# Kernel optimization log

Measured on AMD Instinct MI355X. Metric: run time of the kernel, lower is better.

## Reference

```python
import jax, jax.numpy as jnp
import numpy as np

NUM_NODES = 50000
NUM_EDGES = 640000
IN_FEAT = 128
OUT_FEAT = 128


def setup_inputs() -> dict:
    key = jax.random.key(0)
    k1, k2, k3, k4 = jax.random.split(key, 4)
    features = jax.random.normal(k1, (NUM_NODES, IN_FEAT), dtype=jnp.float32)
    weight = jax.random.normal(k2, (IN_FEAT, OUT_FEAT), dtype=jnp.float32) * (1.0 / np.sqrt(IN_FEAT))
    edges_dst = jax.random.randint(k3, (NUM_EDGES,), 0, NUM_NODES, dtype=jnp.int32)
    edges_src = jax.random.randint(k4, (NUM_EDGES,), 0, NUM_NODES, dtype=jnp.int32)
    return {"features": features, "weight": weight, "edges_dst": edges_dst, "edges_src": edges_src}


def reference(features, weight, edges_dst, edges_src):
    # nodes_representation = features @ W   -> [N, out_feat]
    nodes_representation = jnp.matmul(features, weight)

    # gather neighbor (source) features: [E, in_feat]
    neighbour = features[edges_src]

    # unsorted_segment_mean over target node ids (edges_dst)
    seg_sum = jax.ops.segment_sum(neighbour, edges_dst, num_segments=NUM_NODES)
    counts = jax.ops.segment_sum(jnp.ones((NUM_EDGES,), dtype=features.dtype),
                                 edges_dst, num_segments=NUM_NODES)
    aggregated = jnp.where(counts[:, None] > 0, seg_sum / jnp.maximum(counts[:, None], 1.0), 0.0)

    aggregated_messages = jnp.matmul(aggregated, weight)  # [N, out_feat]

    # combination_type == 'concat', activation == 'relu'
    h = jnp.concatenate([nodes_representation, aggregated_messages], axis=-1)  # [N, 2*out_feat]
    return jax.nn.relu(h)
```

## Files before the change

### kernel.cpp

```cpp
#include <hip/hip_runtime.h>

#define FEAT 128
#define CAP 64
#define SCAT_BLK 192

typedef __attribute__((ext_vector_type(8))) short bhalf8;
typedef __attribute__((ext_vector_type(4))) float floatx4;

__device__ __forceinline__ unsigned short f2bf(float f) {
    unsigned int u = __float_as_uint(f);
    unsigned int r = (u + 0x7fffu + ((u >> 16) & 1u)) >> 16;
    return (unsigned short)r;
}

#define SB_STRIDE 136
__global__ __launch_bounds__(256, 4) void fused_kernel(
    const float* __restrict__ feat, const float* __restrict__ W,
    unsigned short* __restrict__ P2, float* __restrict__ out, int nrows,
    const int* __restrict__ edst, const int* __restrict__ esrc,
    int* __restrict__ counts, int* __restrict__ bucket, int nE)
{
    __shared__ unsigned short sB[128 * SB_STRIDE];

    const int tid = threadIdx.x;

    if (blockIdx.x < SCAT_BLK) {
        const int nE4 = nE >> 2;
        const int gthreads = SCAT_BLK * 256;
        for (int g = blockIdx.x * 256 + tid; g < nE4; g += gthreads) {
            int4 d = *(const int4*)&edst[g << 2];
            int4 s = *(const int4*)&esrc[g << 2];
            int p;
            p = atomicAdd(&counts[d.x], 1); if (p < CAP) bucket[d.x * CAP + p] = s.x;
            p = atomicAdd(&counts[d.y], 1); if (p < CAP) bucket[d.y * CAP + p] = s.y;
            p = atomicAdd(&counts[d.z], 1); if (p < CAP) bucket[d.z * CAP + p] = s.z;
            p = atomicAdd(&counts[d.w], 1); if (p < CAP) bucket[d.w * CAP + p] = s.w;
        }
        if (blockIdx.x == 0 && tid == 0) {
            for (int i = nE4 << 2; i < nE; ++i) {
                int p = atomicAdd(&counts[edst[i]], 1);
                if (p < CAP) bucket[edst[i] * CAP + p] = esrc[i];
            }
        }
        return;
    }

    const int bx   = blockIdx.x - SCAT_BLK;
    const int wave = tid >> 6;
    const int lane = tid & 63;
    const int m    = lane & 15;
    const int kg   = lane >> 4;

    for (int i = tid; i < 2048; i += 256) {
        int n  = i & 127;
        int kc = i >> 7;
        unsigned short tmp[8];
        #pragma unroll
        for (int t = 0; t < 8; ++t)
            tmp[t] = f2bf(W[(size_t)(kc * 8 + t) * FEAT + n]);
        *(uint4*)&sB[n * SB_STRIDE + kc * 8] = *(uint4*)tmp;
    }

    const int row  = bx * 64 + wave * 16 + m;
    const int rowc = min(row, nrows - 1);
    bhalf8 afrag[4];
    {
        const float* ap = &feat[(size_t)rowc * FEAT + kg * 8];
        #pragma unroll
        for (int ks = 0; ks < 4; ++ks) {
            float4 f0 = *(const float4*)&ap[ks * 32];
            float4 f1 = *(const float4*)&ap[ks * 32 + 4];
            union { bhalf8 v; unsigned short u[8]; } a;
            a.u[0] = f2bf(f0.x); a.u[1] = f2bf(f0.y);
            a.u[2] = f2bf(f0.z); a.u[3] = f2bf(f0.w);
            a.u[4] = f2bf(f1.x); a.u[5] = f2bf(f1.y);
            a.u[6] = f2bf(f1.z); a.u[7] = f2bf(f1.w);
            afrag[ks] = a.v;
        }
    }

    __syncthreads();

    floatx4 acc[8];
    #pragma unroll
    for (int nt = 0; nt < 8; ++nt) acc[nt] = (floatx4){0.f, 0.f, 0.f, 0.f};

    #pragma unroll
    for (int ks = 0; ks < 4; ++ks) {
        #pragma unroll
        for (int nt = 0; nt < 8; ++nt) {
            bhalf8 b = *(bhalf8*)&sB[(nt * 16 + m) * SB_STRIDE + ks * 32 + kg * 8];
            acc[nt] = __builtin_amdgcn_mfma_f32_16x16x32_bf16(afrag[ks], b, acc[nt], 0, 0, 0);
        }
    }

    const int rbase = bx * 64 + wave * 16 + kg * 4;
    #pragma unroll
    for (int i = 0; i < 4; ++i) {
        int r = rbase + i;
        if (r < nrows) {
            #pragma unroll
            for (int nt = 0; nt < 8; ++nt) {
                float v = acc[nt][i];
                int c = nt * 16 + m;
                out[(size_t)r * (2 * FEAT) + c] = fmaxf(v, 0.f);
                P2[(size_t)r * FEAT + c] = f2bf(v);
            }
        }
    }
}

__global__ __launch_bounds__(256) void aggregate_kernel(
    const unsigned short* __restrict__ P2, const int* __restrict__ counts,
    const int* __restrict__ bucket, float* __restrict__ out, int n)
{
    const int node = blockIdx.x * 4 + (threadIdx.x >> 6);
    if (node >= n) return;
    const int lane = threadIdx.x & 63;
    const int g  = lane >> 4;
    const int cl = lane & 15;

    const int deg = min(counts[node], CAP);

    float a[8];
    #pragma unroll
    for (int t = 0; t < 8; ++t) a[t] = 0.f;

    int myIdx = (lane < deg) ? bucket[node * CAP + lane] : 0;

    #pragma unroll 4
    for (int j = 0; j < deg; j += 4) {
        int s = __shfl(myIdx, j + g);
        if (j + g < deg) {
            uint4 v = *(const uint4*)&P2[(size_t)s * FEAT + cl * 8];
            a[0] += __uint_as_float(v.x << 16);
            a[1] += __uint_as_float(v.x & 0xffff0000u);
            a[2] += __uint_as_float(v.y << 16);
            a[3] += __uint_as_float(v.y & 0xffff0000u);
            a[4] += __uint_as_float(v.z << 16);
            a[5] += __uint_as_float(v.z & 0xffff0000u);
            a[6] += __uint_as_float(v.w << 16);
            a[7] += __uint_as_float(v.w & 0xffff0000u);
        }
    }

    #pragma unroll
    for (int t = 0; t < 8; ++t) {
        a[t] += __shfl_xor(a[t], 16);
        a[t] += __shfl_xor(a[t], 32);
    }

    if (g == 0) {
        const float inv = (deg > 0) ? (1.0f / (float)deg) : 0.0f;
        float4 r0 = make_float4(fmaxf(a[0] * inv, 0.f), fmaxf(a[1] * inv, 0.f),
                                fmaxf(a[2] * inv, 0.f), fmaxf(a[3] * inv, 0.f));
        float4 r1 = make_float4(fmaxf(a[4] * inv, 0.f), fmaxf(a[5] * inv, 0.f),
                                fmaxf(a[6] * inv, 0.f), fmaxf(a[7] * inv, 0.f));
        float* op = &out[(size_t)node * (2 * FEAT) + FEAT + cl * 8];
        *(float4*)op = r0;
        *(float4*)(op + 4) = r1;
    }
}

extern "C" void kernel_launch(void* const* d_in, const int* in_sizes, int n_in,
                              void* d_out, int out_size, void* d_ws, size_t ws_size,
                              hipStream_t stream)
{
    const float* feat = (const float*)d_in[0];
    const float* W    = (const float*)d_in[1];
    const int* edst   = (const int*)d_in[2];
    const int* esrc   = (const int*)d_in[3];
    float* out        = (float*)d_out;

    const int N = in_sizes[0] / FEAT;
    const int E = in_sizes[2];

    char* ws = (char*)d_ws;
    unsigned short* P2 = (unsigned short*)ws;
    size_t off = (size_t)N * FEAT * sizeof(unsigned short);
    off = (off + 15) & ~(size_t)15;
    int* counts = (int*)(ws + off); off += (size_t)N * 4;
    off = (off + 15) & ~(size_t)15;
    int* bucket = (int*)(ws + off); off += (size_t)N * CAP * 4;

    hipMemsetAsync(counts, 0, (size_t)N * 4, stream);

    const int gemmBlocks = (N + 63) / 64;
    fused_kernel<<<SCAT_BLK + gemmBlocks, 256, 0, stream>>>(
        feat, W, P2, out, N, edst, esrc, counts, bucket, E);

    aggregate_kernel<<<(N + 3) / 4, 256, 0, stream>>>(P2, counts, bucket, out, N);
}
```

Before: 150.7 us.

## Replace global atomic edge scatter with per-block LDS binning over node ranges

Each binning block now owns a contiguous range of 196 destination nodes. It scans the full edge list, builds counts and source buckets in LDS using shared-memory atomics, then writes them out to global memory with vectorized stores. This removes the contended global atomics, the scattered bucket writes and the counts memset. In exchange, every binning block rereads the whole destination array, so total L2 traffic grows with the number of blocks. The larger shared allocation, now also reserved by the GEMM blocks, may lower occupancy.

```diff
diff --git a/kernel.cpp b/kernel.cpp
--- a/kernel.cpp
+++ b/kernel.cpp
@@ -2,7 +2,8 @@
 
 #define FEAT 128
 #define CAP 64
-#define SCAT_BLK 192
+#define NPB 196
+#define SB_STRIDE 136
 
 typedef __attribute__((ext_vector_type(8))) short bhalf8;
 typedef __attribute__((ext_vector_type(4))) float floatx4;
@@ -13,39 +14,61 @@
     return (unsigned short)r;
 }
 
-#define SB_STRIDE 136
 __global__ __launch_bounds__(256, 4) void fused_kernel(
     const float* __restrict__ feat, const float* __restrict__ W,
     unsigned short* __restrict__ P2, float* __restrict__ out, int nrows,
     const int* __restrict__ edst, const int* __restrict__ esrc,
-    int* __restrict__ counts, int* __restrict__ bucket, int nE)
+    int* __restrict__ counts, int* __restrict__ bucket, int nE, int binBlocks)
 {
-    __shared__ unsigned short sB[128 * SB_STRIDE];
+    __shared__ int4 smem4[(NPB + NPB * CAP) / 4 + 1];
+    int* smem = (int*)smem4;
 
     const int tid = threadIdx.x;
 
-    if (blockIdx.x < SCAT_BLK) {
+    if ((int)blockIdx.x < binBlocks) {
+        int* cnt = smem;
+        int* bkt = smem + NPB;
+        const int base = blockIdx.x * NPB;
+        const unsigned int span = (unsigned int)min(NPB, nrows - base);
+
+        for (int i = tid; i < NPB; i += 256) cnt[i] = 0;
+        __syncthreads();
+
         const int nE4 = nE >> 2;
-        const int gthreads = SCAT_BLK * 256;
-        for (int g = blockIdx.x * 256 + tid; g < nE4; g += gthreads) {
+        for (int g = tid; g < nE4; g += 256) {
             int4 d = *(const int4*)&edst[g << 2];
-            int4 s = *(const int4*)&esrc[g << 2];
-            int p;
-            p = atomicAdd(&counts[d.x], 1); if (p < CAP) bucket[d.x * CAP + p] = s.x;
-            p = atomicAdd(&counts[d.y], 1); if (p < CAP) bucket[d.y * CAP + p] = s.y;
-            p = atomicAdd(&counts[d.z], 1); if (p < CAP) bucket[d.z * CAP + p] = s.z;
-            p = atomicAdd(&counts[d.w], 1); if (p < CAP) bucket[d.w * CAP + p] = s.w;
-        }
-        if (blockIdx.x == 0 && tid == 0) {
-            for (int i = nE4 << 2; i < nE; ++i) {
-                int p = atomicAdd(&counts[edst[i]], 1);
-                if (p < CAP) bucket[edst[i] * CAP + p] = esrc[i];
+            unsigned int l;
+            l = (unsigned int)(d.x - base);
+            if (l < span) { int s = atomicAdd(&cnt[l], 1); if (s < CAP) bkt[l * CAP + s] = esrc[(g << 2) + 0]; }
+            l = (unsigned int)(d.y - base);
+            if (l < span) { int s = atomicAdd(&cnt[l], 1); if (s < CAP) bkt[l * CAP + s] = esrc[(g << 2) + 1]; }
+            l = (unsigned int)(d.z - base);
+            if (l < span) { int s = atomicAdd(&cnt[l], 1); if (s < CAP) bkt[l * CAP + s] = esrc[(g << 2) + 2]; }
+            l = (unsigned int)(d.w - base);
+            if (l < span) { int s = atomicAdd(&cnt[l], 1); if (s < CAP) bkt[l * CAP + s] = esrc[(g << 2) + 3]; }
+        }
+        if (blockIdx.x == 0) {
+            for (int i = (nE4 << 2) + tid; i < nE; i += 256) {
             }
         }
+        for (int i = (nE4 << 2) + tid; i < nE; i += 256) {
+            unsigned int l = (unsigned int)(edst[i] - base);
+            if (l < span) { int s = atomicAdd(&cnt[l], 1); if (s < CAP) bkt[l * CAP + s] = esrc[i]; }
+        }
+        __syncthreads();
+
+        for (int i = tid; i < (int)span; i += 256) counts[base + i] = cnt[i];
+        for (int idx = tid; idx < (int)span * (CAP / 4); idx += 256) {
+            int nl = idx >> 4;
+            int q  = idx & 15;
+            if (q * 4 < min(cnt[nl], CAP))
+                *(int4*)&bucket[(size_t)(base + nl) * CAP + q * 4] = *(int4*)&bkt[nl * CAP + q * 4];
+        }
         return;
     }
 
-    const int bx   = blockIdx.x - SCAT_BLK;
+    unsigned short* sB = (unsigned short*)smem;
+    const int bx   = blockIdx.x - binBlocks;
     const int wave = tid >> 6;
     const int lane = tid & 63;
     const int m    = lane & 15;
@@ -183,11 +206,11 @@
     off = (off + 15) & ~(size_t)15;
     int* bucket = (int*)(ws + off); off += (size_t)N * CAP * 4;
 
-    hipMemsetAsync(counts, 0, (size_t)N * 4, stream);
-
+    const int binBlocks  = (N + NPB - 1) / NPB;
     const int gemmBlocks = (N + 63) / 64;
-    fused_kernel<<<SCAT_BLK + gemmBlocks, 256, 0, stream>>>(
-        feat, W, P2, out, N, edst, esrc, counts, bucket, E);
+
+    fused_kernel<<<binBlocks + gemmBlocks, 256, 0, stream>>>(
+        feat, W, P2, out, N, edst, esrc, counts, bucket, E, binBlocks);
 
     aggregate_kernel<<<(N + 3) / 4, 256, 0, stream>>>(P2, counts, bucket, out, N);
 }
```

Measured after the change: 372.5 us. 147% more time.
